# Kernel tuning notes

Hardware: AMD Instinct MI355X
Metric: run time of the kernel (lower is better)

Reference implementation:

```python
import jax, jax.numpy as jnp
import numpy as np

EPS_NORM = 1e-5   # instance-norm epsilon (NormalizeLayer over spatial axes)
EPS_VAR = 1e-9    # floor used before sqrt, as in the original


def _instance_norm(x):
    # normalize over spatial axes (1,2), per batch & channel
    mean = jnp.mean(x, axis=(1, 2), keepdims=True)
    var = jnp.var(x, axis=(1, 2), keepdims=True)
    return (x - mean) * jax.lax.rsqrt(var + EPS_NORM)


def _aat(content, style, comb_c, comb_s):
    # content/style: (B,H,W,C); comb_*: (B,H,W,Cc)
    B, H, W, C = content.shape
    N = H * W
    norm_content = _instance_norm(content)
    q = _instance_norm(comb_c).reshape(B, N, -1)   # (B,N,Cc)
    k = _instance_norm(comb_s).reshape(B, N, -1)   # (B,N,Cc)
    v = style.reshape(B, N, C)                     # (B,N,C)
    scores = jnp.einsum('bnc,bmc->bnm', q, k)      # Q_T @ K
    A = jax.nn.softmax(scores, axis=-1)            # (B,N,N)
    M = jnp.einsum('bnm,bmc->bnc', A, v)           # weighted mean
    S2 = jnp.einsum('bnm,bmc->bnc', A, v * v) - M * M  # weighted variance
    S = jnp.sqrt(jnp.maximum(jax.nn.relu(S2), EPS_VAR))
    S = S.reshape(B, H, W, C)
    M = M.reshape(B, H, W, C)
    return S * norm_content + M


def _feature_loss(cs, c, s, cc, sc):
    aat = _aat(c, s, cc, sc)
    return jnp.mean(jnp.square(cs - aat))


def setup_inputs() -> dict:
    key = jax.random.key(0)
    shapes = {
        'cs2': (4, 64, 64, 256), 'c2': (4, 64, 64, 256), 's2': (4, 64, 64, 256),
        'cc2': (4, 64, 64, 448), 'sc2': (4, 64, 64, 448),
        'cs3': (4, 32, 32, 512), 'c3': (4, 32, 32, 512), 's3': (4, 32, 32, 512),
        'cc3': (4, 32, 32, 960), 'sc3': (4, 32, 32, 960),
        'cs4': (4, 16, 16, 512), 'c4': (4, 16, 16, 512), 's4': (4, 16, 16, 512),
        'cc4': (4, 16, 16, 1472), 'sc4': (4, 16, 16, 1472),
    }
    keys = jax.random.split(key, len(shapes))
    return {name: jax.random.normal(k, shp, dtype=jnp.float32)
            for k, (name, shp) in zip(keys, shapes.items())}


def reference(cs2, c2, s2, cc2, sc2, cs3, c3, s3, cc3, sc3, cs4, c4, s4, cc4, sc4):
    loss = _feature_loss(cs2, c2, s2, cc2, sc2)
    loss = loss + _feature_loss(cs3, c3, s3, cc3, sc3)
    loss = loss + _feature_loss(cs4, c4, s4, cc4, sc4)
    return loss
```

## Files before the change

kernel.cpp:

```cpp
#include <hip/hip_runtime.h>
#include <math.h>

#define EPS_NORM 1e-5f
#define EPS_VAR  1e-9f
#define LOG2E    1.4426950408889634f

typedef unsigned short ushort_t;
typedef __attribute__((ext_vector_type(4))) float f32x4;
typedef _Float16 half8 __attribute__((ext_vector_type(8)));

#define MFMAH(a, b, c) __builtin_amdgcn_mfma_f32_16x16x32_f16((a), (b), (c), 0, 0, 0)

#define GLD16(gp, lp) __builtin_amdgcn_global_load_lds(                          \
    (const __attribute__((address_space(1))) unsigned int*)(gp),                 \
    (__attribute__((address_space(3))) unsigned int*)(lp), 16, 0, 0)

__device__ inline ushort_t f16_bits(float x) {
    _Float16 h = (_Float16)x;
    ushort_t u;
    __builtin_memcpy(&u, &h, 2);
    return u;
}
__device__ inline half8 ldh(const ushort_t* p) {
    half8 h;
    __builtin_memcpy(&h, p, 16);
    return h;
}
__device__ inline uint4 pack8(const ushort_t* s) {
    uint4 r;
    r.x = (unsigned)s[0] | ((unsigned)s[1] << 16);
    r.y = (unsigned)s[2] | ((unsigned)s[3] << 16);
    r.z = (unsigned)s[4] | ((unsigned)s[5] << 16);
    r.w = (unsigned)s[6] | ((unsigned)s[7] << 16);
    return r;
}

struct StatJobs {
    const float* x[9];
    float* sm[9];
    float* sq[9];
    int N[9], Cn[9], chG[9], nG[9], base[9];
};
__global__ void __launch_bounds__(256) stat_partial_all(StatJobs J)
{
    int bx = blockIdx.x;
    int j = 0;
#pragma unroll
    for (int k = 1; k < 9; ++k) if (bx >= J.base[k]) j = k;
    bx -= J.base[j];
    const int N = J.N[j], Cn = J.Cn[j], chG = J.chG[j], nG = J.nG[j];
    int b  = bx / (chG * nG);
    int r  = bx % (chG * nG);
    int cg = r / nG;
    int ng = r % nG;
    int ch = cg * 256 + threadIdx.x;
    if (ch >= Cn) return;
    int n0 = ng * 256;
    int n1 = min(n0 + 256, N);
    const float* p = J.x[j] + (long)(b * N) * Cn + ch;
    float s = 0.f, ss = 0.f;
    for (int n = n0; n < n1; ++n) {
        float v = p[(long)n * Cn];
        s += v;
        ss = fmaf(v, v, ss);
    }
    atomicAdd(&J.sm[j][b * Cn + ch], s);
    atomicAdd(&J.sq[j][b * Cn + ch], ss);
}

struct FinJobs {
    float* sm[9];
    float* sq[9];
    int base[9];
    float invN[9];
    int total;
};
__global__ void __launch_bounds__(256) stat_finalize_all(FinJobs J)
{
    int i = blockIdx.x * 256 + threadIdx.x;
    if (i >= J.total) return;
    int j = 0;
#pragma unroll
    for (int k = 1; k < 9; ++k) if (i >= J.base[k]) j = k;
    int e = i - J.base[j];
    float m = J.sm[j][e] * J.invN[j];
    float v = J.sq[j][e] * J.invN[j] - m * m;
    J.sm[j][e] = m;
    J.sq[j][e] = rsqrtf(v + EPS_NORM);
}

struct PrepJobs {
    const float* qx[3]; const float* qm[3]; const float* qr[3]; ushort_t* qh[3];
    const float* kx[3]; const float* km[3]; const float* kr[3]; ushort_t* kh[3];
    const float* vx[3]; ushort_t* vt[3];
    int N[3], Cc[3], C[3], KSEG[3], nbase[3];
};
__global__ void __launch_bounds__(256) prep_all(PrepJobs J)
{
    int bx = blockIdx.x;
    int j = 0;
#pragma unroll
    for (int k = 1; k < 3; ++k) if (bx >= J.nbase[k]) j = k;
    bx -= J.nbase[j];
    const int N = J.N[j], Cc = J.Cc[j];
    const int normBlocks = 2 * N;
    if (bx < normBlocks) {
        const int wave = threadIdx.x >> 6, lane = threadIdx.x & 63;
        int rr = bx * 4 + wave;
        const int BN = 4 * N;
        const bool isQ = rr < BN;
        int bn = isQ ? rr : rr - BN;
        const float* x    = isQ ? J.qx[j] : J.kx[j];
        const float* mean = isQ ? J.qm[j] : J.km[j];
        const float* rstd = isQ ? J.qr[j] : J.kr[j];
        ushort_t* out     = isQ ? J.qh[j] : J.kh[j];
        const float scl   = isQ ? LOG2E : 1.0f;
        int b = bn / N;
        long base = (long)bn * Cc;
        const float* mb = mean + b * Cc;
        const float* rb = rstd + b * Cc;
        for (int c8 = lane; c8 * 8 < Cc; c8 += 64) {
            int ch = c8 * 8;
            float4 a0 = *(const float4*)(x + base + ch);
            float4 a1 = *(const float4*)(x + base + ch + 4);
            float4 m0 = *(const float4*)(mb + ch);
            float4 m1 = *(const float4*)(mb + ch + 4);
            float4 r0 = *(const float4*)(rb + ch);
            float4 r1 = *(const float4*)(rb + ch + 4);
            ushort_t h8[8];
            h8[0] = f16_bits((a0.x - m0.x) * r0.x * scl);
            h8[1] = f16_bits((a0.y - m0.y) * r0.y * scl);
            h8[2] = f16_bits((a0.z - m0.z) * r0.z * scl);
            h8[3] = f16_bits((a0.w - m0.w) * r0.w * scl);
            h8[4] = f16_bits((a1.x - m1.x) * r1.x * scl);
            h8[5] = f16_bits((a1.y - m1.y) * r1.y * scl);
            h8[6] = f16_bits((a1.z - m1.z) * r1.z * scl);
            h8[7] = f16_bits((a1.w - m1.w) * r1.w * scl);
            *(uint4*)(out + base + ch) = pack8(h8);
        }
    } else {
        int bid2 = bx - normBlocks;
        const int C = J.C[j], KSEG = J.KSEG[j];
        const float* vx = J.vx[j];
        ushort_t* vt = J.vt[j];
        int cPB = C / 64, nSeg = N / KSEG;
        int b   = bid2 / (cPB * nSeg);
        int rem = bid2 % (cPB * nSeg);
        int cb  = rem / nSeg;
        int ns  = rem % nSeg;
        int ch  = cb * 64 + (threadIdx.x & 63);
        const int KL = KSEG / 4;
        int k0  = ns * KSEG + (threadIdx.x >> 6) * KL;
        long obase = ((long)b * C + ch) * N;
        for (int k = k0; k < k0 + KL; k += 8) {
            ushort_t h8[8];
#pragma unroll
            for (int i = 0; i < 8; ++i)
                h8[i] = f16_bits(vx[((long)b * N + k + i) * C + ch]);
            *(uint4*)(vt + obase + k) = pack8(h8);
        }
    }
}

__device__ inline void stage64_async(const ushort_t* __restrict__ g, long rowBase,
                                     int gstride, int col0, ushort_t* slab, int tid)
{
    const int l  = tid & 63, w = tid >> 6;
    const int rs = l >> 3;
    const int cg = (l & 7) ^ rs;
#pragma unroll
    for (int i = 0; i < 2; ++i) {
        const int r = w * 16 + i * 8 + rs;
        const ushort_t* gp = g + (rowBase + r) * (long)gstride + col0 + (cg << 3);
        ushort_t* lp = slab + (w * 16 + i * 8) * 64 + l * 8;
        GLD16(gp, lp);
    }
}
template<int BROWS>
__device__ inline void stageQ_async(const ushort_t* __restrict__ g, long rowBase,
                                    int gstride, int col0, ushort_t* slab, int tid)
{
    if (tid < BROWS * 8) {
        const int l  = tid & 63, w = tid >> 6;
        const int rs = l >> 3;
        const int cg = (l & 7) ^ rs;
        const int r  = w * 8 + rs;
        const ushort_t* gp = g + (rowBase + r) * (long)gstride + col0 + (cg << 3);
        ushort_t* lp = slab + w * 8 * 64 + l * 8;
        GLD16(gp, lp);
    }
}
__device__ inline half8 ldsw(const ushort_t* slab, int row, int soff)
{
    const int gr = (soff >> 3) ^ (row & 7);
    return ldh(slab + row * 64 + (gr << 3));
}

__global__ void __launch_bounds__(256, 2) flash_pipe(
    const ushort_t* __restrict__ Qh, const ushort_t* __restrict__ Kh,
    const ushort_t* __restrict__ Vth,
    float* __restrict__ Pmo, float* __restrict__ Plo,
    float* __restrict__ PMo, float* __restrict__ PSo)
{
    constexpr int Cc = 448, C = 256, N = 4096, SPLIT = 2;
    constexpr int NKT  = (N / 64) / SPLIT;
    constexpr long VCHO = 64L * N;
    constexpr long KADV = 64L * Cc;

    __shared__ __align__(16) ushort_t smem[4 * 8192 + 4 * 1152];
    const int tid  = threadIdx.x;
    const int lane = tid & 63;
    const int w    = tid >> 6;
    const int l15  = lane & 15;
    const int quad = lane >> 4;

    const int bq = blockIdx.x / SPLIT;
    const int sp = blockIdx.x % SPLIT;
    const int b  = bq / (N / 64);
    const int qb = bq % (N / 64);
    const int i0 = qb * 64 + w * 16;
    const long po = (long)(b * (N / 16) + qb * 4 + w) * SPLIT + sp;

    const int rs    = lane >> 3;
    const int cg    = (lane & 7) ^ rs;
    const int ldso0 = w * 1024 + lane * 8;
    const int ldso1 = ldso0 + 512;
    const int xh    = l15 & 7;
    const int lb0   = l15 * 64 + ((quad)     ^ xh) * 8;
    const int lb1   = l15 * 64 + ((4 + quad) ^ xh) * 8;
    ushort_t* const Pw  = smem + 32768 + w * 1152;
    ushort_t* const pww = Pw + quad * 288 + l15;
    const ushort_t* const pfr = Pw + l15 * 72 + quad * 8;

    const long krow0 = (long)b * N + (long)sp * NKT * 64;
    const ushort_t* kp0 = Kh + (krow0 + w * 16 + rs) * (long)Cc + (cg << 3);
    const ushort_t* kp1 = kp0 + 8 * Cc;
    const ushort_t* vp0 = Vth + ((long)b * C + w * 16 + rs) * (long)N
                              + (cg << 3) + (long)sp * NKT * 64;
    const ushort_t* vp1 = vp0 + 8 * (long)N;

#define SLOT(k) (smem + (k) * 8192)
#define STGKP(c0, c1, slot, toff) do {                                           \
    GLD16(kp0 + (toff) + (c0) * 64, SLOT(slot) + ldso0);                         \
    GLD16(kp1 + (toff) + (c0) * 64, SLOT(slot) + ldso1);                         \
    GLD16(kp0 + (toff) + (c1) * 64, SLOT(slot) + 4096 + ldso0);                  \
    GLD16(kp1 + (toff) + (c1) * 64, SLOT(slot) + 4096 + ldso1); } while (0)
#define STGK1(c0, slot, toff) do {                                               \
    GLD16(kp0 + (toff) + (c0) * 64, SLOT(slot) + ldso0);                         \
    GLD16(kp1 + (toff) + (c0) * 64, SLOT(slot) + ldso1); } while (0)
#define STGVP(j0, slot, voff) do {                                               \
    GLD16(vp0 + (voff) + (j0) * VCHO, SLOT(slot) + ldso0);                       \
    GLD16(vp1 + (voff) + (j0) * VCHO, SLOT(slot) + ldso1);                       \
    GLD16(vp0 + (voff) + ((j0) + 1) * VCHO, SLOT(slot) + 4096 + ldso0);          \
    GLD16(vp1 + (voff) + ((j0) + 1) * VCHO, SLOT(slot) + 4096 + ldso1); } while (0)

#define WAITV(NN) asm volatile("s_waitcnt vmcnt(" #NN ")" ::: "memory");         \
    __builtin_amdgcn_sched_barrier(0);                                           \
    __builtin_amdgcn_s_barrier();                                                \
    __builtin_amdgcn_s_setprio(1);
#define PH_END __builtin_amdgcn_s_setprio(0);

#define QKPAIR(slot, c0) do {                                                    \
    const ushort_t* s0_ = SLOT(slot);                                            \
    const ushort_t* s1_ = s0_ + 4096;                                            \
    _Pragma("unroll")                                                            \
    for (int ct = 0; ct < 4; ++ct) S[ct] = MFMAH(qf[2*(c0)+0], ldh(s0_ + ct*1024 + lb0), S[ct]); \
    _Pragma("unroll")                                                            \
    for (int ct = 0; ct < 4; ++ct) S[ct] = MFMAH(qf[2*(c0)+1], ldh(s0_ + ct*1024 + lb1), S[ct]); \
    _Pragma("unroll")                                                            \
    for (int ct = 0; ct < 4; ++ct) S[ct] = MFMAH(qf[2*(c0)+2], ldh(s1_ + ct*1024 + lb0), S[ct]); \
    _Pragma("unroll")                                                            \
    for (int ct = 0; ct < 4; ++ct) S[ct] = MFMAH(qf[2*(c0)+3], ldh(s1_ + ct*1024 + lb1), S[ct]); } while (0)
#define QK1(slot, c0) do {                                                       \
    const ushort_t* s0_ = SLOT(slot);                                            \
    _Pragma("unroll")                                                            \
    for (int ct = 0; ct < 4; ++ct) S[ct] = MFMAH(qf[2*(c0)+0], ldh(s0_ + ct*1024 + lb0), S[ct]); \
    _Pragma("unroll")                                                            \
    for (int ct = 0; ct < 4; ++ct) S[ct] = MFMAH(qf[2*(c0)+1], ldh(s0_ + ct*1024 + lb1), S[ct]); } while (0)
#define PVPAIR(slot, ci0) do {                                                   \
    const ushort_t* s0_ = SLOT(slot);                                            \
    const ushort_t* s1_ = s0_ + 4096;                                            \
    _Pragma("unroll")                                                            \
    for (int ct = 0; ct < 4; ++ct) {                                             \
        half8 vh = ldh(s0_ + ct*1024 + lb0); half8 uh = vh * vh;                 \
        Mac[(ci0)*4 + ct] = MFMAH(pf0, vh, Mac[(ci0)*4 + ct]);                   \
        Sac[(ci0)*4 + ct] = MFMAH(pf0, uh, Sac[(ci0)*4 + ct]); }                 \
    _Pragma("unroll")                                                            \
    for (int ct = 0; ct < 4; ++ct) {                                             \
        half8 vh = ldh(s0_ + ct*1024 + lb1); half8 uh = vh * vh;                 \
        Mac[(ci0)*4 + ct] = MFMAH(pf1, vh, Mac[(ci0)*4 + ct]);                   \
        Sac[(ci0)*4 + ct] = MFMAH(pf1, uh, Sac[(ci0)*4 + ct]); }                 \
    _Pragma("unroll")                                                            \
    for (int ct = 0; ct < 4; ++ct) {                                             \
        half8 vh = ldh(s1_ + ct*1024 + lb0); half8 uh = vh * vh;                 \
        Mac[(ci0+1)*4 + ct] = MFMAH(pf0, vh, Mac[(ci0+1)*4 + ct]);               \
        Sac[(ci0+1)*4 + ct] = MFMAH(pf0, uh, Sac[(ci0+1)*4 + ct]); }             \
    _Pragma("unroll")                                                            \
    for (int ct = 0; ct < 4; ++ct) {                                             \
        half8 vh = ldh(s1_ + ct*1024 + lb1); half8 uh = vh * vh;                 \
        Mac[(ci0+1)*4 + ct] = MFMAH(pf1, vh, Mac[(ci0+1)*4 + ct]);               \
        Sac[(ci0+1)*4 + ct] = MFMAH(pf1, uh, Sac[(ci0+1)*4 + ct]); } } while (0)
#define RESET_S do {                                                             \
    _Pragma("unroll")                                                            \
    for (int ct = 0; ct < 4; ++ct)                                               \
        _Pragma("unroll")                                                        \
        for (int r = 0; r < 4; ++r) S[ct][r] = 0.f; } while (0)

    half8 qf[14];
    {
        const ushort_t* q1 = Qh + ((long)(b * N + i0 + l15)) * Cc + quad * 8;
#pragma unroll
        for (int ks = 0; ks < 14; ++ks) qf[ks] = ldh(q1 + ks * 32);
    }
    asm volatile("s_waitcnt vmcnt(0)" ::: "memory");

    float m_r[4], l_l[4], mw = -1e30f;
    f32x4 Mac[16], Sac[16];
    f32x4 S[4];
    half8 pf0, pf1;
#pragma unroll
    for (int r = 0; r < 4; ++r) { m_r[r] = -1e30f; l_l[r] = 0.f; }
#pragma unroll
    for (int ct = 0; ct < 16; ++ct)
#pragma unroll
        for (int r = 0; r < 4; ++r) { Mac[ct][r] = 0.f; Sac[ct][r] = 0.f; }

    auto softmax_step = [&]() {
        float tmax = S[0][0];
#pragma unroll
        for (int ct = 0; ct < 4; ++ct)
#pragma unroll
            for (int r = 0; r < 4; ++r) tmax = fmaxf(tmax, S[ct][r]);
#pragma unroll
        for (int off = 1; off <= 32; off <<= 1)
            tmax = fmaxf(tmax, __shfl_xor(tmax, off, 64));

        if (tmax > mw + 14.4269504f) {
            float rm[4];
#pragma unroll
            for (int r = 0; r < 4; ++r)
                rm[r] = fmaxf(fmaxf(S[0][r], S[1][r]), fmaxf(S[2][r], S[3][r]));
#pragma unroll
            for (int off = 1; off <= 8; off <<= 1)
#pragma unroll
                for (int r = 0; r < 4; ++r)
                    rm[r] = fmaxf(rm[r], __shfl_xor(rm[r], off, 64));
#pragma unroll
            for (int r = 0; r < 4; ++r) {
                float mn = fmaxf(m_r[r], rm[r]);
                float corr = exp2f(m_r[r] - mn);
                m_r[r] = mn;
                l_l[r] *= corr;
#pragma unroll
                for (int ct = 0; ct < 16; ++ct) { Mac[ct][r] *= corr; Sac[ct][r] *= corr; }
            }
            float tt = fminf(fminf(m_r[0], m_r[1]), fminf(m_r[2], m_r[3]));
            tt = fminf(tt, __shfl_xor(tt, 16, 64));
            tt = fminf(tt, __shfl_xor(tt, 32, 64));
            mw = tt;
        }
#pragma unroll
        for (int ct = 0; ct < 4; ++ct)
#pragma unroll
            for (int r = 0; r < 4; ++r) {
                float p = exp2f(S[ct][r] - m_r[r]);
                l_l[r] += p;
                pww[r * 72 + ct * 16] = f16_bits(p);
            }
        pf0 = ldh(pfr);
        pf1 = ldh(pfr + 32);
    };

    STGKP(0, 1, 0, 0);
    STGKP(2, 3, 1, 0);

    for (int it = 0; it < NKT / 2; ++it) {
        RESET_S;
        STGKP(4, 5, 2, 0);
        WAITV(8)  QKPAIR(0, 0); PH_END;
        STGK1(6, 3, 0);
        WAITV(6)  QKPAIR(1, 2); PH_END;
        STGVP(0, 0, 0);
        WAITV(6)  QKPAIR(2, 4); PH_END;
        STGVP(2, 1, 0);
        WAITV(8)  QK1(3, 6); PH_END;
        softmax_step();
        STGKP(0, 1, 2, KADV);
        WAITV(8)  PVPAIR(0, 0); PH_END;
        STGKP(2, 3, 3, KADV);
        WAITV(8)  PVPAIR(1, 2); PH_END;

        RESET_S;
        STGKP(4, 5, 0, KADV);
        WAITV(8)  QKPAIR(2, 0); PH_END;
        STGK1(6, 1, KADV);
        WAITV(6)  QKPAIR(3, 2); PH_END;
        STGVP(0, 2, 64);
        WAITV(6)  QKPAIR(0, 4); PH_END;
        STGVP(2, 3, 64);
        WAITV(8)  QK1(1, 6); PH_END;
        softmax_step();
        const bool more = (it + 1 < NKT / 2);
        if (more) {
            kp0 += 2 * KADV; kp1 += 2 * KADV;
            STGKP(0, 1, 0, 0);
            asm volatile("s_waitcnt vmcnt(8)" ::: "memory");
        } else {
            asm volatile("s_waitcnt vmcnt(4)" ::: "memory");
        }
        __builtin_amdgcn_sched_barrier(0);
        __builtin_amdgcn_s_barrier();
        __builtin_amdgcn_s_setprio(1);
        PVPAIR(2, 0);
        PH_END;
        if (more) {
            STGKP(2, 3, 1, 0);
            asm volatile("s_waitcnt vmcnt(8)" ::: "memory");
        } else {
            asm volatile("s_waitcnt vmcnt(0)" ::: "memory");
        }
        __builtin_amdgcn_sched_barrier(0);
        __builtin_amdgcn_s_barrier();
        __builtin_amdgcn_s_setprio(1);
        PVPAIR(3, 2);
        PH_END;

        vp0 += 128; vp1 += 128;
    }
#undef SLOT
#undef STGKP
#undef STGK1
#undef STGVP
#undef WAITV
#undef PH_END
#undef QKPAIR
#undef QK1
#undef PVPAIR
#undef RESET_S

#pragma unroll
    for (int off = 1; off <= 8; off <<= 1)
#pragma unroll
        for (int r = 0; r < 4; ++r) l_l[r] += __shfl_xor(l_l[r], off, 64);

    if (l15 == 0) {
#pragma unroll
        for (int r = 0; r < 4; ++r) {
            Pmo[po * 16 + quad * 4 + r] = m_r[r];
            Plo[po * 16 + quad * 4 + r] = l_l[r];
        }
    }
#pragma unroll
    for (int ct = 0; ct < 16; ++ct)
#pragma unroll
        for (int r = 0; r < 4; ++r) {
            long idx = (po * 16 + quad * 4 + r) * C + ct * 16 + l15;
            PMo[idx] = Mac[ct][r];
            PSo[idx] = Sac[ct][r];
        }
}

template<int Cc, int C, int N, int CSPLIT, bool QREG, int SPLIT, int SLABS, int KGRP>
__global__ void __launch_bounds__(256, 2) flash_mfma(
    const ushort_t* __restrict__ Qh, const ushort_t* __restrict__ Kh,
    const ushort_t* __restrict__ Vth,
    float* __restrict__ Pmo, float* __restrict__ Plo,
    float* __restrict__ PMo, float* __restrict__ PSo)
{
    constexpr int KC      = Cc / 64;
    constexpr int VC      = C / 64;
    constexpr int VCW     = VC / CSPLIT;
    constexpr int CTCW    = 4 * VCW;
    constexpr int STRIPES = 4 / CSPLIT;
    constexpr int BROWS   = 16 * STRIPES;
    constexpr int QB      = N / BROWS;
    constexpr int TILES   = N / 64;
    constexpr int NKT     = TILES / SPLIT;
    constexpr int NKS     = QREG ? (Cc / 32) : 1;
    constexpr int NGRP    = (KC + KGRP - 1) / KGRP;
    constexpr int G       = 4 / CSPLIT;
    constexpr int QCH     = BROWS * 64;
    constexpr int QOFF    = KGRP * 4096;
    constexpr int KQEND   = QOFF + KGRP * QCH;
    constexpr int REGION  = QREG ? (SLABS * 4096)
                                 : (KQEND > SLABS * 4096 ? KQEND : SLABS * 4096);

    __shared__ __align__(16) ushort_t smem[REGION + 4 * 1152];
    const int tid  = threadIdx.x;
    const int lane = tid & 63;
    const int w    = tid >> 6;
    const int l15  = lane & 15;
    const int quad = lane >> 4;

    const int bq = blockIdx.x / SPLIT;
    const int sp = blockIdx.x % SPLIT;
    const int b  = bq / QB;
    const int qb = bq % QB;
    const int ls  = w / CSPLIT;
    const int ch2 = w % CSPLIT;
    const int i0 = qb * BROWS + ls * 16;
    const long po = (long)(b * (N / 16) + qb * STRIPES + ls) * SPLIT + sp;
    ushort_t* Pw = smem + REGION + w * 1152;

    half8 qf[NKS];
    if constexpr (QREG) {
        const ushort_t* q1 = Qh + ((long)(b * N + i0 + l15)) * Cc + quad * 8;
#pragma unroll
        for (int ks = 0; ks < NKS; ++ks) qf[ks] = ldh(q1 + ks * 32);
    }

    float m_r[4], l_l[4], mw = -1e30f;
    f32x4 Mac[CTCW], Sac[CTCW];
#pragma unroll
    for (int r = 0; r < 4; ++r) { m_r[r] = -1e30f; l_l[r] = 0.f; }
#pragma unroll
    for (int ct = 0; ct < CTCW; ++ct)
#pragma unroll
        for (int r = 0; r < 4; ++r) { Mac[ct][r] = 0.f; Sac[ct][r] = 0.f; }

    for (int kt = sp * NKT; kt < sp * NKT + NKT; ++kt) {
        const long krow = (long)b * N + kt * 64;

        f32x4 S[4];
#pragma unroll
        for (int ct = 0; ct < 4; ++ct)
#pragma unroll
            for (int r = 0; r < 4; ++r) S[ct][r] = 0.f;

#pragma unroll
        for (int grp = 0; grp < NGRP; ++grp) {
            const int g0 = grp * KGRP;
            const int gn = (KC - g0 < KGRP) ? (KC - g0) : KGRP;
            __syncthreads();
#pragma unroll
            for (int j = 0; j < KGRP; ++j) if (j < gn) {
                stage64_async(Kh, krow, Cc, (g0 + j) * 64, smem + j * 4096, tid);
                if constexpr (!QREG)
                    stageQ_async<BROWS>(Qh, (long)b * N + qb * BROWS, Cc, (g0 + j) * 64,
                                        smem + QOFF + j * QCH, tid);
            }
            __syncthreads();
#pragma unroll
            for (int j = 0; j < KGRP; ++j) if (j < gn) {
#pragma unroll
                for (int ks = 0; ks < 2; ++ks) {
                    half8 a;
                    if constexpr (QREG) a = qf[(g0 + j) * 2 + ks];
                    else a = ldsw(smem + QOFF + j * QCH, ls * 16 + l15, ks * 32 + quad * 8);
#pragma unroll
                    for (int ct = 0; ct < 4; ++ct) {
                        half8 bf = ldsw(smem + j * 4096, ct * 16 + l15, ks * 32 + quad * 8);
                        S[ct] = MFMAH(a, bf, S[ct]);
                    }
                }
            }
        }

        float tmax = S[0][0];
#pragma unroll
        for (int ct = 0; ct < 4; ++ct)
#pragma unroll
            for (int r = 0; r < 4; ++r) tmax = fmaxf(tmax, S[ct][r]);
#pragma unroll
        for (int off = 1; off <= 32; off <<= 1)
            tmax = fmaxf(tmax, __shfl_xor(tmax, off, 64));

        if (tmax > mw + 14.4269504f) {
            float rm[4];
#pragma unroll
            for (int r = 0; r < 4; ++r)
                rm[r] = fmaxf(fmaxf(S[0][r], S[1][r]), fmaxf(S[2][r], S[3][r]));
#pragma unroll
            for (int off = 1; off <= 8; off <<= 1)
#pragma unroll
                for (int r = 0; r < 4; ++r)
                    rm[r] = fmaxf(rm[r], __shfl_xor(rm[r], off, 64));
#pragma unroll
            for (int r = 0; r < 4; ++r) {
                float mn = fmaxf(m_r[r], rm[r]);
                float corr = exp2f(m_r[r] - mn);
                m_r[r] = mn;
                l_l[r] *= corr;
#pragma unroll
                for (int ct = 0; ct < CTCW; ++ct) { Mac[ct][r] *= corr; Sac[ct][r] *= corr; }
            }
            float t = fminf(fminf(m_r[0], m_r[1]), fminf(m_r[2], m_r[3]));
            t = fminf(t, __shfl_xor(t, 16, 64));
            t = fminf(t, __shfl_xor(t, 32, 64));
            mw = t;
        }

#pragma unroll
        for (int ct = 0; ct < 4; ++ct)
#pragma unroll
            for (int r = 0; r < 4; ++r) {
                float p = exp2f(S[ct][r] - m_r[r]);
                l_l[r] += p;
                Pw[(quad * 4 + r) * 72 + ct * 16 + l15] = f16_bits(p);
            }

        half8 pf0 = ldh(Pw + l15 * 72 + 0  + quad * 8);
        half8 pf1 = ldh(Pw + l15 * 72 + 32 + quad * 8);

#pragma unroll
        for (int g = 0; g < VCW; g += G) {
            __syncthreads();
#pragma unroll
            for (int s = 0; s < 4; ++s) {
                const int h = s / G, j = s % G;
                stage64_async(Vth, (long)b * C + (h * VCW + g + j) * 64, N, kt * 64,
                              smem + s * 4096, tid);
            }
            __syncthreads();
#pragma unroll
            for (int ks = 0; ks < 2; ++ks) {
                half8 pf = ks ? pf1 : pf0;
#pragma unroll
                for (int j = 0; j < G; ++j)
#pragma unroll
                    for (int ct = 0; ct < 4; ++ct) {
                        half8 vh = ldsw(smem + (ch2 * G + j) * 4096,
                                        ct * 16 + l15, ks * 32 + quad * 8);
                        half8 uh = vh * vh;
                        const int ci = (g + j) * 4 + ct;
                        Mac[ci] = MFMAH(pf, vh, Mac[ci]);
                        Sac[ci] = MFMAH(pf, uh, Sac[ci]);
                    }
            }
        }
    }

#pragma unroll
    for (int off = 1; off <= 8; off <<= 1)
#pragma unroll
        for (int r = 0; r < 4; ++r) l_l[r] += __shfl_xor(l_l[r], off, 64);

    if (ch2 == 0 && l15 == 0) {
#pragma unroll
        for (int r = 0; r < 4; ++r) {
            Pmo[po * 16 + quad * 4 + r] = m_r[r];
            Plo[po * 16 + quad * 4 + r] = l_l[r];
        }
    }
    const int chb = ch2 * (C / CSPLIT);
#pragma unroll
    for (int ct = 0; ct < CTCW; ++ct)
#pragma unroll
        for (int r = 0; r < 4; ++r) {
            long idx = (po * 16 + quad * 4 + r) * C + chb + ct * 16 + l15;
            PMo[idx] = Mac[ct][r];
            PSo[idx] = Sac[ct][r];
        }
}

template<int C, int SPLIT>
__global__ void __launch_bounds__(256) combine_aat(
    const float* __restrict__ Pm, const float* __restrict__ Pl,
    const float* __restrict__ PM, const float* __restrict__ PS,
    const float* __restrict__ CT, const float* __restrict__ CS,
    const float* __restrict__ cmean, const float* __restrict__ crstd,
    float* __restrict__ loss, int N)
{
    constexpr int CL4 = C / 4;
    __shared__ float wS[SPLIT][16];
    __shared__ float invL[16];
    __shared__ float red[4];
    const int pi = blockIdx.x;
    const int nb = N / 16;
    const int b  = pi / nb;
    const long g0 = (long)b * N + (long)(pi % nb) * 16;
    const int tid = threadIdx.x;

    if (tid < 16) {
        float m = -1e30f;
#pragma unroll
        for (int s = 0; s < SPLIT; ++s)
            m = fmaxf(m, Pm[((long)pi * SPLIT + s) * 16 + tid]);
        float L = 0.f;
#pragma unroll
        for (int s = 0; s < SPLIT; ++s) {
            float e = exp2f(Pm[((long)pi * SPLIT + s) * 16 + tid] - m);
            wS[s][tid] = e;
            L = fmaf(e, Pl[((long)pi * SPLIT + s) * 16 + tid], L);
        }
        invL[tid] = 1.f / L;
    }
    __syncthreads();

    float acc = 0.f;
    for (int v = tid; v < 4 * C; v += 256) {
        const int r  = v / CL4;
        const int c0 = (v - r * CL4) * 4;
        const long q0 = (((long)pi * SPLIT) * 16 + r) * C + c0;
        float4 Ms = {0.f, 0.f, 0.f, 0.f}, Ss = {0.f, 0.f, 0.f, 0.f};
#pragma unroll
        for (int s = 0; s < SPLIT; ++s) {
            const float ws_ = wS[s][r];
            const float4 pm = *(const float4*)&PM[q0 + (long)s * 16 * C];
            const float4 ps = *(const float4*)&PS[q0 + (long)s * 16 * C];
            Ms.x = fmaf(ws_, pm.x, Ms.x); Ms.y = fmaf(ws_, pm.y, Ms.y);
            Ms.z = fmaf(ws_, pm.z, Ms.z); Ms.w = fmaf(ws_, pm.w, Ms.w);
            Ss.x = fmaf(ws_, ps.x, Ss.x); Ss.y = fmaf(ws_, ps.y, Ss.y);
            Ss.z = fmaf(ws_, ps.z, Ss.z); Ss.w = fmaf(ws_, ps.w, Ss.w);
        }
        const float iL = invL[r];
        const float4 ctv = *(const float4*)&CT[(g0 + r) * C + c0];
        const float4 csv = *(const float4*)&CS[(g0 + r) * C + c0];
        const float4 cmv = *(const float4*)&cmean[b * C + c0];
        const float4 crv = *(const float4*)&crstd[b * C + c0];
#pragma unroll
        for (int e = 0; e < 4; ++e) {
            const float Msx = (&Ms.x)[e] * iL;
            const float S2  = (&Ss.x)[e] * iL - Msx * Msx;
            const float Sx  = sqrtf(fmaxf(S2, EPS_VAR));
            const float nc  = ((&ctv.x)[e] - (&cmv.x)[e]) * (&crv.x)[e];
            const float d   = (&csv.x)[e] - (Sx * nc + Msx);
            acc = fmaf(d, d, acc);
        }
    }
#pragma unroll
    for (int off = 1; off <= 32; off <<= 1) acc += __shfl_xor(acc, off, 64);
    if ((tid & 63) == 0) red[tid >> 6] = acc;
    __syncthreads();
    if (tid == 0) atomicAdd(loss, red[0] + red[1] + red[2] + red[3]);
}

template<int CCL, int CL, int NQ>
__global__ void __launch_bounds__(256) flash_aat(
    const float* __restrict__ Q, const float* __restrict__ K, const float* __restrict__ V,
    const float* __restrict__ CT, const float* __restrict__ CS,
    const float* __restrict__ qmean, const float* __restrict__ qrstd,
    const float* __restrict__ kmean, const float* __restrict__ krstd,
    const float* __restrict__ cmean, const float* __restrict__ crstd,
    float* __restrict__ loss, int N)
{
    constexpr int CC   = CCL * 64;
    constexpr int C    = CL * 64;
    constexpr int ROWS = 4 * NQ;
    const int lane = threadIdx.x & 63;
    const int wave = threadIdx.x >> 6;
    const int rowBlocks = N / ROWS;
    const int b  = blockIdx.x / rowBlocks;
    const int rb = blockIdx.x % rowBlocks;
    const int i0 = rb * ROWS + wave * NQ;

    float kmu[CCL], krs[CCL];
#pragma unroll
    for (int t = 0; t < CCL; ++t) {
        int ch = lane + 64 * t;
        kmu[t] = kmean[b * CC + ch];
        krs[t] = krstd[b * CC + ch];
    }
    float q[NQ][CCL];
#pragma unroll
    for (int qi = 0; qi < NQ; ++qi) {
        long base = (long)(b * N + i0 + qi) * CC;
#pragma unroll
        for (int t = 0; t < CCL; ++t) {
            int ch = lane + 64 * t;
            q[qi][t] = (Q[base + ch] - qmean[b * CC + ch]) * qrstd[b * CC + ch];
        }
    }
    float mval[NQ], lsum[NQ];
    float Macc[NQ][CL], Sacc[NQ][CL];
#pragma unroll
    for (int qi = 0; qi < NQ; ++qi) {
        mval[qi] = -1e30f; lsum[qi] = 0.f;
#pragma unroll
        for (int t = 0; t < CL; ++t) { Macc[qi][t] = 0.f; Sacc[qi][t] = 0.f; }
    }
    for (int j = 0; j < N; ++j) {
        long kb = (long)(b * N + j) * CC;
        float dot[NQ];
#pragma unroll
        for (int qi = 0; qi < NQ; ++qi) dot[qi] = 0.f;
#pragma unroll
        for (int t = 0; t < CCL; ++t) {
            float kv = (K[kb + lane + 64 * t] - kmu[t]) * krs[t];
#pragma unroll
            for (int qi = 0; qi < NQ; ++qi) dot[qi] = fmaf(q[qi][t], kv, dot[qi]);
        }
#pragma unroll
        for (int off = 32; off > 0; off >>= 1)
#pragma unroll
            for (int qi = 0; qi < NQ; ++qi) dot[qi] += __shfl_xor(dot[qi], off, 64);
        long vb = (long)(b * N + j) * C;
        float vv[CL];
#pragma unroll
        for (int t = 0; t < CL; ++t) vv[t] = V[vb + lane + 64 * t];
#pragma unroll
        for (int qi = 0; qi < NQ; ++qi) {
            float s = dot[qi];
            float p;
            if (s > mval[qi]) {
                float cr2 = __expf(mval[qi] - s);
                lsum[qi] *= cr2;
#pragma unroll
                for (int t = 0; t < CL; ++t) { Macc[qi][t] *= cr2; Sacc[qi][t] *= cr2; }
                mval[qi] = s; p = 1.f;
            } else p = __expf(s - mval[qi]);
            lsum[qi] += p;
#pragma unroll
            for (int t = 0; t < CL; ++t) {
                float pv = p * vv[t];
                Macc[qi][t] += pv;
                Sacc[qi][t] = fmaf(pv, vv[t], Sacc[qi][t]);
            }
        }
    }
    float acc = 0.f;
#pragma unroll
    for (int qi = 0; qi < NQ; ++qi) {
        float inv_l = 1.f / lsum[qi];
        long base = (long)(b * N + i0 + qi) * C;
#pragma unroll
        for (int t = 0; t < CL; ++t) {
            int ch = lane + 64 * t;
            float M  = Macc[qi][t] * inv_l;
            float S2 = Sacc[qi][t] * inv_l - M * M;
            float S  = sqrtf(fmaxf(S2, EPS_VAR));
            float nc = (CT[base + ch] - cmean[b * C + ch]) * crstd[b * C + ch];
            float d  = CS[base + ch] - (S * nc + M);
            acc = fmaf(d, d, acc);
        }
    }
#pragma unroll
    for (int off = 32; off > 0; off >>= 1) acc += __shfl_xor(acc, off, 64);
    if (lane == 0) atomicAdd(loss, acc);
}

__global__ void combine_loss(const float* __restrict__ lp, float* __restrict__ out,
                             float s0, float s1, float s2)
{
    out[0] = lp[0] * s0 + lp[1] * s1 + lp[2] * s2;
}

extern "C" void kernel_launch(void* const* d_in, const int* in_sizes, int n_in,
                              void* d_out, int out_size, void* d_ws, size_t ws_size,
                              hipStream_t stream)
{
    const float* cs2 = (const float*)d_in[0];
    const float* c2  = (const float*)d_in[1];
    const float* s2v = (const float*)d_in[2];
    const float* cc2 = (const float*)d_in[3];
    const float* sc2 = (const float*)d_in[4];
    const float* cs3 = (const float*)d_in[5];
    const float* c3  = (const float*)d_in[6];
    const float* s3v = (const float*)d_in[7];
    const float* cc3 = (const float*)d_in[8];
    const float* sc3 = (const float*)d_in[9];
    const float* cs4 = (const float*)d_in[10];
    const float* c4  = (const float*)d_in[11];
    const float* s4v = (const float*)d_in[12];
    const float* cc4 = (const float*)d_in[13];
    const float* sc4 = (const float*)d_in[14];

    const int B = 4;
    float* ws = (float*)d_ws;
    size_t fo = 0;
    auto allocF = [&](size_t n) { float* p = ws + fo; fo += n; return p; };

    float* lossp = allocF(4);
    float* c2m = allocF(B * 256);  float* c2r = allocF(B * 256);
    float* q2m = allocF(B * 448);  float* q2r = allocF(B * 448);
    float* k2m = allocF(B * 448);  float* k2r = allocF(B * 448);
    float* c3m = allocF(B * 512);  float* c3r = allocF(B * 512);
    float* q3m = allocF(B * 960);  float* q3r = allocF(B * 960);
    float* k3m = allocF(B * 960);  float* k3r = allocF(B * 960);
    float* c4m = allocF(B * 512);  float* c4r = allocF(B * 512);
    float* q4m = allocF(B * 1472); float* q4r = allocF(B * 1472);
    float* k4m = allocF(B * 1472); float* k4r = allocF(B * 1472);
    size_t zeroBytes = fo * sizeof(float);

    float* Pm = allocF(32768);
    float* Pl = allocF(32768);
    float* PM = allocF(8388608);
    float* PS = allocF(8388608);

    size_t arenaOff = ((fo * 4 + 15) & ~(size_t)15) / 2;
    ushort_t* arena = (ushort_t*)d_ws + arenaOff;
    const size_t arenaShorts = 18874400;
    size_t need = arenaOff * 2 + arenaShorts * 2;
    const bool fast = (ws_size >= need);

    hipMemsetAsync(d_ws, 0, zeroBytes, stream);

    {
        StatJobs SJ; FinJobs FJ;
        const float* xs[9] = {c2, cc2, sc2, c3, cc3, sc3, c4, cc4, sc4};
        float* sms[9] = {c2m, q2m, k2m, c3m, q3m, k3m, c4m, q4m, k4m};
        float* sqs[9] = {c2r, q2r, k2r, c3r, q3r, k3r, c4r, q4r, k4r};
        const int Ns[9]  = {4096, 4096, 4096, 1024, 1024, 1024, 256, 256, 256};
        const int Cns[9] = {256, 448, 448, 512, 960, 960, 512, 1472, 1472};
        int pb = 0, fb = 0;
        for (int j = 0; j < 9; ++j) {
            int chG = (Cns[j] + 255) / 256;
            int nG  = (Ns[j] + 255) / 256;
            SJ.x[j] = xs[j]; SJ.sm[j] = sms[j]; SJ.sq[j] = sqs[j];
            SJ.N[j] = Ns[j]; SJ.Cn[j] = Cns[j]; SJ.chG[j] = chG; SJ.nG[j] = nG;
            SJ.base[j] = pb;
            pb += B * chG * nG;
            FJ.sm[j] = sms[j]; FJ.sq[j] = sqs[j]; FJ.base[j] = fb;
            FJ.invN[j] = 1.0f / (float)Ns[j];
            fb += B * Cns[j];
        }
        FJ.total = fb;
        hipLaunchKernelGGL(stat_partial_all, dim3(pb), dim3(256), 0, stream, SJ);
        hipLaunchKernelGGL(stat_finalize_all, dim3((fb + 255) / 256), dim3(256), 0, stream, FJ);
    }

    if (fast) {
        auto arenaFor = [&](size_t& o, size_t n) {
            ushort_t* p = arena + o; o += (n + 7) & ~(size_t)7; return p;
        };
        size_t o2 = 0;
        ushort_t* qh2 = arenaFor(o2, (size_t)B*4096*448);
        ushort_t* kh2 = arenaFor(o2, (size_t)B*4096*448);
        ushort_t* vh2 = arenaFor(o2, (size_t)B*4096*256);
        size_t o3 = 0;
        ushort_t* qh3 = arenaFor(o3, (size_t)B*1024*960);
        ushort_t* kh3 = arenaFor(o3, (size_t)B*1024*960);
        ushort_t* vh3 = arenaFor(o3, (size_t)B*1024*512);
        size_t o4 = 0;
        ushort_t* qh4 = arenaFor(o4, (size_t)B*256*1472);
        ushort_t* kh4 = arenaFor(o4, (size_t)B*256*1472);
        ushort_t* vh4 = arenaFor(o4, (size_t)B*256*512);

        size_t totShorts = o2 + o3 + o4;
        bool prepFused = (ws_size >= arenaOff * 2 + totShorts * 2);
        if (prepFused) {
            qh3 = arena + o2;        kh3 = qh3 + (((size_t)B*1024*960 + 7) & ~(size_t)7);
            vh3 = kh3 + (((size_t)B*1024*960 + 7) & ~(size_t)7);
            qh4 = arena + o2 + o3;   kh4 = qh4 + (((size_t)B*256*1472 + 7) & ~(size_t)7);
            vh4 = kh4 + (((size_t)B*256*1472 + 7) & ~(size_t)7);

            PrepJobs PJ;
            PJ.qx[0]=cc2; PJ.qm[0]=q2m; PJ.qr[0]=q2r; PJ.qh[0]=qh2;
            PJ.kx[0]=sc2; PJ.km[0]=k2m; PJ.kr[0]=k2r; PJ.kh[0]=kh2;
            PJ.vx[0]=s2v; PJ.vt[0]=vh2; PJ.N[0]=4096; PJ.Cc[0]=448; PJ.C[0]=256; PJ.KSEG[0]=512;
            PJ.qx[1]=cc3; PJ.qm[1]=q3m; PJ.qr[1]=q3r; PJ.qh[1]=qh3;
            PJ.kx[1]=sc3; PJ.km[1]=k3m; PJ.kr[1]=k3r; PJ.kh[1]=kh3;
            PJ.vx[1]=s3v; PJ.vt[1]=vh3; PJ.N[1]=1024; PJ.Cc[1]=960; PJ.C[1]=512; PJ.KSEG[1]=512;
            PJ.qx[2]=cc4; PJ.qm[2]=q4m; PJ.qr[2]=q4r; PJ.qh[2]=qh4;
            PJ.kx[2]=sc4; PJ.km[2]=k4m; PJ.kr[2]=k4r; PJ.kh[2]=kh4;
            PJ.vx[2]=s4v; PJ.vt[2]=vh4; PJ.N[2]=256;  PJ.Cc[2]=1472; PJ.C[2]=512; PJ.KSEG[2]=256;
            int g0n = 2*4096 + B*(256/64)*(4096/512);
            int g1n = 2*1024 + B*(512/64)*(1024/512);
            int g2n = 2*256  + B*(512/64)*(256/256);
            PJ.nbase[0] = 0; PJ.nbase[1] = g0n; PJ.nbase[2] = g0n + g1n;
            hipLaunchKernelGGL(prep_all, dim3(g0n + g1n + g2n), dim3(256), 0, stream, PJ);
        }

        {
            if (!prepFused) {
                PrepJobs PJ;
                PJ.qx[0]=cc2; PJ.qm[0]=q2m; PJ.qr[0]=q2r; PJ.qh[0]=qh2;
                PJ.kx[0]=sc2; PJ.km[0]=k2m; PJ.kr[0]=k2r; PJ.kh[0]=kh2;
                PJ.vx[0]=s2v; PJ.vt[0]=vh2; PJ.N[0]=4096; PJ.Cc[0]=448; PJ.C[0]=256; PJ.KSEG[0]=512;
                for (int k = 1; k < 3; ++k) { PJ.N[k]=4096; PJ.Cc[k]=448; PJ.C[k]=256; PJ.KSEG[k]=512;
                    PJ.qx[k]=cc2; PJ.qm[k]=q2m; PJ.qr[k]=q2r; PJ.qh[k]=qh2;
                    PJ.kx[k]=sc2; PJ.km[k]=k2m; PJ.kr[k]=k2r; PJ.kh[k]=kh2;
                    PJ.vx[k]=s2v; PJ.vt[k]=vh2; }
                int gn = 2*4096 + B*(256/64)*(4096/512);
                PJ.nbase[0]=0; PJ.nbase[1]=gn; PJ.nbase[2]=gn;
                hipLaunchKernelGGL(prep_all, dim3(gn), dim3(256), 0, stream, PJ);
            }
            hipLaunchKernelGGL(flash_pipe, dim3(B*(4096/64)*2), dim3(256), 0, stream,
                               qh2, kh2, vh2, Pm, Pl, PM, PS);
            hipLaunchKernelGGL((combine_aat<256, 2>), dim3(B*4096/16), dim3(256), 0, stream,
                               Pm, Pl, PM, PS, c2, cs2, c2m, c2r, &lossp[0], 4096);
        }
        {
            if (!prepFused) {
                PrepJobs PJ;
                PJ.qx[0]=cc3; PJ.qm[0]=q3m; PJ.qr[0]=q3r; PJ.qh[0]=qh3;
                PJ.kx[0]=sc3; PJ.km[0]=k3m; PJ.kr[0]=k3r; PJ.kh[0]=kh3;
                PJ.vx[0]=s3v; PJ.vt[0]=vh3; PJ.N[0]=1024; PJ.Cc[0]=960; PJ.C[0]=512; PJ.KSEG[0]=512;
                for (int k = 1; k < 3; ++k) { PJ.N[k]=1024; PJ.Cc[k]=960; PJ.C[k]=512; PJ.KSEG[k]=512;
                    PJ.qx[k]=cc3; PJ.qm[k]=q3m; PJ.qr[k]=q3r; PJ.qh[k]=qh3;
                    PJ.kx[k]=sc3; PJ.km[k]=k3m; PJ.kr[k]=k3r; PJ.kh[k]=kh3;
                    PJ.vx[k]=s3v; PJ.vt[k]=vh3; }
                int gn = 2*1024 + B*(512/64)*(1024/512);
                PJ.nbase[0]=0; PJ.nbase[1]=gn; PJ.nbase[2]=gn;
                hipLaunchKernelGGL(prep_all, dim3(gn), dim3(256), 0, stream, PJ);
            }
            hipLaunchKernelGGL((flash_mfma<960, 512, 1024, 2, false, 4, 4, 4>),
                               dim3(B*(1024/32)*4), dim3(256), 0, stream,
                               qh3, kh3, vh3, Pm, Pl, PM, PS);
            hipLaunchKernelGGL((combine_aat<512, 4>), dim3(B*1024/16), dim3(256), 0, stream,
                               Pm, Pl, PM, PS, c3, cs3, c3m, c3r, &lossp[1], 1024);
        }
        {
            if (!prepFused) {
                PrepJobs PJ;
                PJ.qx[0]=cc4; PJ.qm[0]=q4m; PJ.qr[0]=q4r; PJ.qh[0]=qh4;
                PJ.kx[0]=sc4; PJ.km[0]=k4m; PJ.kr[0]=k4r; PJ.kh[0]=kh4;
                PJ.vx[0]=s4v; PJ.vt[0]=vh4; PJ.N[0]=256; PJ.Cc[0]=1472; PJ.C[0]=512; PJ.KSEG[0]=256;
                for (int k = 1; k < 3; ++k) { PJ.N[k]=256; PJ.Cc[k]=1472; PJ.C[k]=512; PJ.KSEG[k]=256;
                    PJ.qx[k]=cc4; PJ.qm[k]=q4m; PJ.qr[k]=q4r; PJ.qh[k]=qh4;
                    PJ.kx[k]=sc4; PJ.km[k]=k4m; PJ.kr[k]=k4r; PJ.kh[k]=kh4;
                    PJ.vx[k]=s4v; PJ.vt[k]=vh4; }
                int gn = 2*256 + B*(512/64)*(256/256);
                PJ.nbase[0]=0; PJ.nbase[1]=gn; PJ.nbase[2]=gn;
                hipLaunchKernelGGL(prep_all, dim3(gn), dim3(256), 0, stream, PJ);
            }
            hipLaunchKernelGGL((flash_mfma<1472, 512, 256, 4, false, 4, 4, 4>),
                               dim3(B*(256/16)*4), dim3(256), 0, stream,
                               qh4, kh4, vh4, Pm, Pl, PM, PS);
            hipLaunchKernelGGL((combine_aat<512, 4>), dim3(B*256/16), dim3(256), 0, stream,
                               Pm, Pl, PM, PS, c4, cs4, c4m, c4r, &lossp[2], 256);
        }
    } else {
        hipLaunchKernelGGL((flash_aat<7, 4, 4>), dim3(B * 4096 / 16), dim3(256), 0, stream,
                           cc2, sc2, s2v, c2, cs2, q2m, q2r, k2m, k2r, c2m, c2r, &lossp[0], 4096);
        hipLaunchKernelGGL((flash_aat<15, 8, 2>), dim3(B * 1024 / 8), dim3(256), 0, stream,
                           cc3, sc3, s3v, c3, cs3, q3m, q3r, k3m, k3r, c3m, c3r, &lossp[1], 1024);
        hipLaunchKernelGGL((flash_aat<23, 8, 2>), dim3(B * 256 / 8), dim3(256), 0, stream,
                           cc4, sc4, s4v, c4, cs4, q4m, q4r, k4m, k4r, c4m, c4r, &lossp[2], 256);
    }

    hipLaunchKernelGGL(combine_loss, dim3(1), dim3(1), 0, stream,
                       lossp, (float*)d_out,
                       1.0f / (4.0f * 4096.0f * 256.0f),
                       1.0f / (4.0f * 1024.0f * 512.0f),
                       1.0f / (4.0f * 256.0f * 512.0f));
}
```

Baseline: 719.2 us.

## Tile V transpose through LDS, remap flash_pipe block order, retune flash template params

The V transpose in prep_all now stages a 64x64 tile in shared memory so the transposed fp16 rows are written as contiguous 16-byte stores instead of strided per-channel writes. flash_pipe's block index mapping is changed so the 8 (batch, split) blocks sharing a query tile are adjacent, which is meant to change L2 locality of K/V reads. The flash_mfma template parameters for levels 3 and 4 are also raised (4,4 to 5,5 and 6,6), likely pipeline or unroll depths. These are independent tweaks, and the larger template values may raise register pressure.

```diff
diff --git a/kernel.cpp b/kernel.cpp
--- a/kernel.cpp
+++ b/kernel.cpp
@@ -93,10 +93,11 @@
     const float* qx[3]; const float* qm[3]; const float* qr[3]; ushort_t* qh[3];
     const float* kx[3]; const float* km[3]; const float* kr[3]; ushort_t* kh[3];
     const float* vx[3]; ushort_t* vt[3];
-    int N[3], Cc[3], C[3], KSEG[3], nbase[3];
+    int N[3], Cc[3], C[3], nbase[3];
 };
 __global__ void __launch_bounds__(256) prep_all(PrepJobs J)
 {
+    __shared__ __align__(16) ushort_t tbuf[64 * 72];
     int bx = blockIdx.x;
     int j = 0;
 #pragma unroll
@@ -140,24 +141,30 @@
         }
     } else {
         int bid2 = bx - normBlocks;
-        const int C = J.C[j], KSEG = J.KSEG[j];
-        const float* vx = J.vx[j];
-        ushort_t* vt = J.vt[j];
-        int cPB = C / 64, nSeg = N / KSEG;
-        int b   = bid2 / (cPB * nSeg);
-        int rem = bid2 % (cPB * nSeg);
-        int cb  = rem / nSeg;
-        int ns  = rem % nSeg;
-        int ch  = cb * 64 + (threadIdx.x & 63);
-        const int KL = KSEG / 4;
-        int k0  = ns * KSEG + (threadIdx.x >> 6) * KL;
-        long obase = ((long)b * C + ch) * N;
-        for (int k = k0; k < k0 + KL; k += 8) {
+        const int C = J.C[j];
+        const int cT = C >> 6, nT = N >> 6;
+        int b   = bid2 / (cT * nT);
+        int rem = bid2 % (cT * nT);
+        int ch0 = (rem / nT) << 6;
+        int n0  = (rem % nT) << 6;
+        const int lane = threadIdx.x & 63, wv = threadIdx.x >> 6;
+        const float* vb_ = J.vx[j] + (long)b * N * C + ch0 + lane;
+#pragma unroll
+        for (int jj = 0; jj < 2; ++jj) {
+            int nl = wv * 16 + jj * 8;
             ushort_t h8[8];
 #pragma unroll
             for (int i = 0; i < 8; ++i)
-                h8[i] = f16_bits(vx[((long)b * N + k + i) * C + ch]);
-            *(uint4*)(vt + obase + k) = pack8(h8);
+                h8[i] = f16_bits(vb_[(long)(n0 + nl + i) * C]);
+            *(uint4*)&tbuf[lane * 72 + nl] = pack8(h8);
+        }
+        __syncthreads();
+        {
+            const int chl = threadIdx.x >> 2;
+            const int nq  = (threadIdx.x & 3) * 16;
+            ushort_t* op = J.vt[j] + ((long)b * C + ch0 + chl) * N + n0 + nq;
+            *(uint4*)op       = *(const uint4*)&tbuf[chl * 72 + nq];
+            *(uint4*)(op + 8) = *(const uint4*)&tbuf[chl * 72 + nq + 8];
         }
     }
 }
@@ -214,10 +221,10 @@
     const int l15  = lane & 15;
     const int quad = lane >> 4;
 
-    const int bq = blockIdx.x / SPLIT;
-    const int sp = blockIdx.x % SPLIT;
-    const int b  = bq / (N / 64);
-    const int qb = bq % (N / 64);
+    const int grp = blockIdx.x & 7;
+    const int sp  = grp & 1;
+    const int b   = grp >> 1;
+    const int qb  = (int)(blockIdx.x >> 3);
     const int i0 = qb * 64 + w * 16;
     const long po = (long)(b * (N / 16) + qb * 4 + w) * SPLIT + sp;
 
@@ -926,6 +933,10 @@
         ushort_t* kh4 = arenaFor(o4, (size_t)B*256*1472);
         ushort_t* vh4 = arenaFor(o4, (size_t)B*256*512);
 
+        const int vt2 = (256/64)*(4096/64)*B;
+        const int vt3 = (512/64)*(1024/64)*B;
+        const int vt4 = (512/64)*(256/64)*B;
+
         size_t totShorts = o2 + o3 + o4;
         bool prepFused = (ws_size >= arenaOff * 2 + totShorts * 2);
         if (prepFused) {
@@ -937,16 +948,16 @@
             PrepJobs PJ;
             PJ.qx[0]=cc2; PJ.qm[0]=q2m; PJ.qr[0]=q2r; PJ.qh[0]=qh2;
             PJ.kx[0]=sc2; PJ.km[0]=k2m; PJ.kr[0]=k2r; PJ.kh[0]=kh2;
-            PJ.vx[0]=s2v; PJ.vt[0]=vh2; PJ.N[0]=4096; PJ.Cc[0]=448; PJ.C[0]=256; PJ.KSEG[0]=512;
+            PJ.vx[0]=s2v; PJ.vt[0]=vh2; PJ.N[0]=4096; PJ.Cc[0]=448; PJ.C[0]=256;
             PJ.qx[1]=cc3; PJ.qm[1]=q3m; PJ.qr[1]=q3r; PJ.qh[1]=qh3;
             PJ.kx[1]=sc3; PJ.km[1]=k3m; PJ.kr[1]=k3r; PJ.kh[1]=kh3;
-            PJ.vx[1]=s3v; PJ.vt[1]=vh3; PJ.N[1]=1024; PJ.Cc[1]=960; PJ.C[1]=512; PJ.KSEG[1]=512;
+            PJ.vx[1]=s3v; PJ.vt[1]=vh3; PJ.N[1]=1024; PJ.Cc[1]=960; PJ.C[1]=512;
             PJ.qx[2]=cc4; PJ.qm[2]=q4m; PJ.qr[2]=q4r; PJ.qh[2]=qh4;
             PJ.kx[2]=sc4; PJ.km[2]=k4m; PJ.kr[2]=k4r; PJ.kh[2]=kh4;
-            PJ.vx[2]=s4v; PJ.vt[2]=vh4; PJ.N[2]=256;  PJ.Cc[2]=1472; PJ.C[2]=512; PJ.KSEG[2]=256;
-            int g0n = 2*4096 + B*(256/64)*(4096/512);
-            int g1n = 2*1024 + B*(512/64)*(1024/512);
-            int g2n = 2*256  + B*(512/64)*(256/256);
+            PJ.vx[2]=s4v; PJ.vt[2]=vh4; PJ.N[2]=256;  PJ.Cc[2]=1472; PJ.C[2]=512;
+            int g0n = 2*4096 + vt2;
+            int g1n = 2*1024 + vt3;
+            int g2n = 2*256  + vt4;
             PJ.nbase[0] = 0; PJ.nbase[1] = g0n; PJ.nbase[2] = g0n + g1n;
             hipLaunchKernelGGL(prep_all, dim3(g0n + g1n + g2n), dim3(256), 0, stream, PJ);
         }
@@ -956,12 +967,12 @@
                 PrepJobs PJ;
                 PJ.qx[0]=cc2; PJ.qm[0]=q2m; PJ.qr[0]=q2r; PJ.qh[0]=qh2;
                 PJ.kx[0]=sc2; PJ.km[0]=k2m; PJ.kr[0]=k2r; PJ.kh[0]=kh2;
-                PJ.vx[0]=s2v; PJ.vt[0]=vh2; PJ.N[0]=4096; PJ.Cc[0]=448; PJ.C[0]=256; PJ.KSEG[0]=512;
-                for (int k = 1; k < 3; ++k) { PJ.N[k]=4096; PJ.Cc[k]=448; PJ.C[k]=256; PJ.KSEG[k]=512;
+                PJ.vx[0]=s2v; PJ.vt[0]=vh2; PJ.N[0]=4096; PJ.Cc[0]=448; PJ.C[0]=256;
+                for (int k = 1; k < 3; ++k) { PJ.N[k]=4096; PJ.Cc[k]=448; PJ.C[k]=256;
                     PJ.qx[k]=cc2; PJ.qm[k]=q2m; PJ.qr[k]=q2r; PJ.qh[k]=qh2;
                     PJ.kx[k]=sc2; PJ.km[k]=k2m; PJ.kr[k]=k2r; PJ.kh[k]=kh2;
                     PJ.vx[k]=s2v; PJ.vt[k]=vh2; }
-                int gn = 2*4096 + B*(256/64)*(4096/512);
+                int gn = 2*4096 + vt2;
                 PJ.nbase[0]=0; PJ.nbase[1]=gn; PJ.nbase[2]=gn;
                 hipLaunchKernelGGL(prep_all, dim3(gn), dim3(256), 0, stream, PJ);
             }
@@ -975,16 +986,16 @@
                 PrepJobs PJ;
                 PJ.qx[0]=cc3; PJ.qm[0]=q3m; PJ.qr[0]=q3r; PJ.qh[0]=qh3;
                 PJ.kx[0]=sc3; PJ.km[0]=k3m; PJ.kr[0]=k3r; PJ.kh[0]=kh3;
-                PJ.vx[0]=s3v; PJ.vt[0]=vh3; PJ.N[0]=1024; PJ.Cc[0]=960; PJ.C[0]=512; PJ.KSEG[0]=512;
-                for (int k = 1; k < 3; ++k) { PJ.N[k]=1024; PJ.Cc[k]=960; PJ.C[k]=512; PJ.KSEG[k]=512;
+                PJ.vx[0]=s3v; PJ.vt[0]=vh3; PJ.N[0]=1024; PJ.Cc[0]=960; PJ.C[0]=512;
+                for (int k = 1; k < 3; ++k) { PJ.N[k]=1024; PJ.Cc[k]=960; PJ.C[k]=512;
                     PJ.qx[k]=cc3; PJ.qm[k]=q3m; PJ.qr[k]=q3r; PJ.qh[k]=qh3;
                     PJ.kx[k]=sc3; PJ.km[k]=k3m; PJ.kr[k]=k3r; PJ.kh[k]=kh3;
                     PJ.vx[k]=s3v; PJ.vt[k]=vh3; }
-                int gn = 2*1024 + B*(512/64)*(1024/512);
+                int gn = 2*1024 + vt3;
                 PJ.nbase[0]=0; PJ.nbase[1]=gn; PJ.nbase[2]=gn;
                 hipLaunchKernelGGL(prep_all, dim3(gn), dim3(256), 0, stream, PJ);
             }
-            hipLaunchKernelGGL((flash_mfma<960, 512, 1024, 2, false, 4, 4, 4>),
+            hipLaunchKernelGGL((flash_mfma<960, 512, 1024, 2, false, 4, 5, 5>),
                                dim3(B*(1024/32)*4), dim3(256), 0, stream,
                                qh3, kh3, vh3, Pm, Pl, PM, PS);
             hipLaunchKernelGGL((combine_aat<512, 4>), dim3(B*1024/16), dim3(256), 0, stream,
@@ -995,16 +1006,16 @@
                 PrepJobs PJ;
                 PJ.qx[0]=cc4; PJ.qm[0]=q4m; PJ.qr[0]=q4r; PJ.qh[0]=qh4;
                 PJ.kx[0]=sc4; PJ.km[0]=k4m; PJ.kr[0]=k4r; PJ.kh[0]=kh4;
-                PJ.vx[0]=s4v; PJ.vt[0]=vh4; PJ.N[0]=256; PJ.Cc[0]=1472; PJ.C[0]=512; PJ.KSEG[0]=256;
-                for (int k = 1; k < 3; ++k) { PJ.N[k]=256; PJ.Cc[k]=1472; PJ.C[k]=512; PJ.KSEG[k]=256;
+                PJ.vx[0]=s4v; PJ.vt[0]=vh4; PJ.N[0]=256; PJ.Cc[0]=1472; PJ.C[0]=512;
+                for (int k = 1; k < 3; ++k) { PJ.N[k]=256; PJ.Cc[k]=1472; PJ.C[k]=512;
                     PJ.qx[k]=cc4; PJ.qm[k]=q4m; PJ.qr[k]=q4r; PJ.qh[k]=qh4;
                     PJ.kx[k]=sc4; PJ.km[k]=k4m; PJ.kr[k]=k4r; PJ.kh[k]=kh4;
                     PJ.vx[k]=s4v; PJ.vt[k]=vh4; }
-                int gn = 2*256 + B*(512/64)*(256/256);
+                int gn = 2*256 + vt4;
                 PJ.nbase[0]=0; PJ.nbase[1]=gn; PJ.nbase[2]=gn;
                 hipLaunchKernelGGL(prep_all, dim3(gn), dim3(256), 0, stream, PJ);
             }
-            hipLaunchKernelGGL((flash_mfma<1472, 512, 256, 4, false, 4, 4, 4>),
+            hipLaunchKernelGGL((flash_mfma<1472, 512, 256, 4, false, 4, 6, 6>),
                                dim3(B*(256/16)*4), dim3(256), 0, stream,
                                qh4, kh4, vh4, Pm, Pl, PM, PS);
             hipLaunchKernelGGL((combine_aat<512, 4>), dim3(B*256/16), dim3(256), 0, stream,
```

After: 682.1 us. 5.2% less time.
